# Kernel optimization log

Measured on AMD Instinct MI355X. Metric: run time of the kernel, lower is better.

The kernel has to match this reference:

```python
import jax, jax.numpy as jnp
import numpy as np

N = 50000       # nodes
E = 600000      # edges (avg degree 12)
F_IN = 64       # input_bands
F_HID = 128     # 2 * input_bands
F_OUT = 128     # output_bands
EPS = 1e-5      # BatchNorm eps


def setup_inputs() -> dict:
    key = jax.random.key(0)
    ks = jax.random.split(key, 12)
    x = jax.random.normal(ks[0], (N, F_IN), jnp.float32)
    edge_index = jax.random.randint(ks[1], (2, E), 0, N, dtype=jnp.int32)
    # GCNConv weight (glorot-ish) and bias
    W1 = jax.random.normal(ks[2], (F_IN, F_HID), jnp.float32) / np.sqrt(F_IN)
    b1 = jnp.zeros((F_HID,), jnp.float32)
    gamma1 = jnp.ones((F_HID,), jnp.float32)
    beta1 = jnp.zeros((F_HID,), jnp.float32)
    # SAGEConv: lin_l (aggregated neighbors, with bias), lin_r (root, no bias)
    Wl = jax.random.normal(ks[3], (F_HID, F_OUT), jnp.float32) / np.sqrt(F_HID)
    bl = jnp.zeros((F_OUT,), jnp.float32)
    Wr = jax.random.normal(ks[4], (F_HID, F_OUT), jnp.float32) / np.sqrt(F_HID)
    gamma2 = jnp.ones((F_OUT,), jnp.float32)
    beta2 = jnp.zeros((F_OUT,), jnp.float32)
    return {"x": x, "edge_index": edge_index, "W1": W1, "b1": b1,
            "gamma1": gamma1, "beta1": beta1, "Wl": Wl, "bl": bl,
            "Wr": Wr, "gamma2": gamma2, "beta2": beta2}


def _bn_train(h, gamma, beta):
    # BatchNorm1d in training mode: biased batch stats over the node axis
    mean = h.mean(axis=0)
    var = h.var(axis=0)
    return gamma * (h - mean) * jax.lax.rsqrt(var + EPS) + beta


def _gcn_conv(x, src, dst, W, b):
    # PyG GCNConv: x' = D^{-1/2}(A + I)D^{-1/2} X W + b
    h = x @ W                                   # [N, F_HID]
    loop = jnp.arange(N, dtype=src.dtype)
    src_sl = jnp.concatenate([src, loop])       # self-loops appended
    dst_sl = jnp.concatenate([dst, loop])
    deg = jax.ops.segment_sum(jnp.ones(E + N, h.dtype), dst_sl, num_segments=N)
    dis = jnp.where(deg > 0, jax.lax.rsqrt(deg), 0.0)  # deg^{-1/2}, inf -> 0
    norm = dis[src_sl] * dis[dst_sl]            # [E+N]
    msg = h[src_sl] * norm[:, None]             # gather + scale
    return jax.ops.segment_sum(msg, dst_sl, num_segments=N) + b


def _sage_conv(x, src, dst, Wl, bl, Wr):
    # PyG SAGEConv (mean aggr): x' = lin_l(mean_{j in N(i)} x_j) + lin_r(x_i)
    cnt = jax.ops.segment_sum(jnp.ones(E, x.dtype), dst, num_segments=N)
    neigh = jax.ops.segment_sum(x[src], dst, num_segments=N)
    neigh = neigh / jnp.maximum(cnt, 1.0)[:, None]
    return neigh @ Wl + bl + x @ Wr


def reference(x, edge_index, W1, b1, gamma1, beta1, Wl, bl, Wr, gamma2, beta2):
    src, dst = edge_index[0], edge_index[1]
    h = _gcn_conv(x, src, dst, W1, b1)
    h = jax.nn.relu(_bn_train(h, gamma1, beta1))  # dropout = identity (eval)
    h = _sage_conv(h, src, dst, Wl, bl, Wr)
    h = jax.nn.relu(_bn_train(h, gamma2, beta2))
    return h
```

## Files before the change

kernel.cpp:

```cpp
#include <hip/hip_runtime.h>

#define NN 50000
#define NE 600000
#define FIN 64
#define FHID 128
#define BN_EPS 1e-5f
#define CAP 64

typedef __attribute__((ext_vector_type(8))) short short8;
typedef __attribute__((ext_vector_type(4))) float f32x4;

__device__ __forceinline__ unsigned short f2bf(float f) {
  unsigned u = __float_as_uint(f);
  return (unsigned short)((u + 0x7FFFu + ((u >> 16) & 1u)) >> 16);
}
__device__ __forceinline__ float bfs(unsigned short u) {
  return __uint_as_float(((unsigned)u) << 16);
}
__device__ __forceinline__ float bflo(unsigned v) { return __uint_as_float(v << 16); }
__device__ __forceinline__ float bfhi(unsigned v) { return __uint_as_float(v & 0xFFFF0000u); }
__device__ __forceinline__ unsigned pk2(float lo, float hi) {
  return (unsigned)f2bf(lo) | ((unsigned)f2bf(hi) << 16);
}

__global__ __launch_bounds__(256) void bucket_fill(const int* __restrict__ src,
                                                   const int* __restrict__ dst,
                                                   int* __restrict__ cnt,
                                                   int* __restrict__ csr) {
  int e4 = blockIdx.x * 256 + threadIdx.x;
  if (e4 * 4 < NE) {
    int4 d4 = ((const int4*)dst)[e4];
    int4 s4 = ((const int4*)src)[e4];
    int p;
    p = atomicAdd(&cnt[d4.x], 1); if (p < CAP) csr[(size_t)d4.x * CAP + p] = s4.x;
    p = atomicAdd(&cnt[d4.y], 1); if (p < CAP) csr[(size_t)d4.y * CAP + p] = s4.y;
    p = atomicAdd(&cnt[d4.z], 1); if (p < CAP) csr[(size_t)d4.z * CAP + p] = s4.z;
    p = atomicAdd(&cnt[d4.w], 1); if (p < CAP) csr[(size_t)d4.w * CAP + p] = s4.w;
  }
}

__global__ __launch_bounds__(256) void scale_x(const float* __restrict__ x,
                                               const int* __restrict__ cnt,
                                               ushort4* __restrict__ xs,
                                               int* __restrict__ csr) {
  int i = blockIdx.x * 256 + threadIdx.x;
  float4 v = ((const float4*)x)[i];
  int node = i >> 4;
  float d = rsqrtf((float)(cnt[node] + 1));
  xs[i] = make_ushort4(f2bf(v.x * d), f2bf(v.y * d), f2bf(v.z * d), f2bf(v.w * d));
  if (i < NN) {
    int deg = min(cnt[i], CAP);
    int deg8 = (deg + 7) & ~7;
    int* cb = csr + (size_t)i * CAP;
    for (int p = deg; p < deg8; ++p) cb[p] = 0;
  }
}

__device__ __forceinline__ void gacc(float& a0, float& a1, float& a2, float& a3,
                                     ushort4 v) {
  a0 += bfs(v.x); a1 += bfs(v.y); a2 += bfs(v.z); a3 += bfs(v.w);
}

__global__ __launch_bounds__(256) void gcn_agg(const unsigned short* __restrict__ xs,
                                               const int* __restrict__ csr,
                                               const int* __restrict__ cnt,
                                               unsigned short* __restrict__ xa) {
  int tid = threadIdx.x;
  int node = blockIdx.x * 16 + (tid >> 4);
  int li = tid & 15;
  int degr = cnt[node];
  int deg = min(degr, CAP);
  int deg8 = (deg + 7) & ~7;
  float di = rsqrtf((float)(degr + 1));
  ushort4 sv = *(const ushort4*)(xs + (size_t)node * FIN + li * 4);
  float a0 = bfs(sv.x), a1 = bfs(sv.y), a2 = bfs(sv.z), a3 = bfs(sv.w);
  ushort4 zv = *(const ushort4*)(xs + li * 4);
  const int* cb = csr + (size_t)node * CAP;
  int4 sA = *(const int4*)(cb);
  int4 sB = *(const int4*)(cb + 4);
  for (int e = 0; e < deg8; e += 8) {
    int pn = min(e + 8, CAP - 8);
    int4 nA = *(const int4*)(cb + pn);
    int4 nB = *(const int4*)(cb + pn + 4);
    ushort4 v0 = *(const ushort4*)(xs + (size_t)sA.x * FIN + li * 4);
    ushort4 v1 = *(const ushort4*)(xs + (size_t)sA.y * FIN + li * 4);
    ushort4 v2 = *(const ushort4*)(xs + (size_t)sA.z * FIN + li * 4);
    ushort4 v3 = *(const ushort4*)(xs + (size_t)sA.w * FIN + li * 4);
    ushort4 v4 = *(const ushort4*)(xs + (size_t)sB.x * FIN + li * 4);
    ushort4 v5 = *(const ushort4*)(xs + (size_t)sB.y * FIN + li * 4);
    ushort4 v6 = *(const ushort4*)(xs + (size_t)sB.z * FIN + li * 4);
    ushort4 v7 = *(const ushort4*)(xs + (size_t)sB.w * FIN + li * 4);
    gacc(a0, a1, a2, a3, v0); gacc(a0, a1, a2, a3, v1);
    gacc(a0, a1, a2, a3, v2); gacc(a0, a1, a2, a3, v3);
    gacc(a0, a1, a2, a3, v4); gacc(a0, a1, a2, a3, v5);
    gacc(a0, a1, a2, a3, v6); gacc(a0, a1, a2, a3, v7);
    sA = nA; sB = nB;
  }
  float pc = (float)(deg8 - deg);
  a0 -= pc * bfs(zv.x); a1 -= pc * bfs(zv.y);
  a2 -= pc * bfs(zv.z); a3 -= pc * bfs(zv.w);
  ushort4 o = make_ushort4(f2bf(di * a0), f2bf(di * a1), f2bf(di * a2), f2bf(di * a3));
  *(ushort4*)(xa + (size_t)node * FIN + li * 4) = o;
}

__device__ __forceinline__ void sacc(float* a, uint4 v) {
  a[0] += bflo(v.x); a[1] += bfhi(v.x);
  a[2] += bflo(v.y); a[3] += bfhi(v.y);
  a[4] += bflo(v.z); a[5] += bfhi(v.z);
  a[6] += bflo(v.w); a[7] += bfhi(v.w);
}

__global__ __launch_bounds__(256) void sage_agg(const unsigned* __restrict__ hb,
                                                const int* __restrict__ csr,
                                                const int* __restrict__ cnt,
                                                unsigned* __restrict__ neighb) {
  int tid = threadIdx.x;
  int node = blockIdx.x * 16 + (tid >> 4);
  int li = tid & 15;
  int degr = cnt[node];
  int deg = min(degr, CAP);
  int deg8 = (deg + 7) & ~7;
  float a[8];
#pragma unroll
  for (int i = 0; i < 8; ++i) a[i] = 0.f;
  uint4 zv = *(const uint4*)(hb + li * 4);
  const int* cb = csr + (size_t)node * CAP;
  int4 sA = *(const int4*)(cb);
  int4 sB = *(const int4*)(cb + 4);
  for (int e = 0; e < deg8; e += 8) {
    int pn = min(e + 8, CAP - 8);
    int4 nA = *(const int4*)(cb + pn);
    int4 nB = *(const int4*)(cb + pn + 4);
    uint4 v0 = *(const uint4*)(hb + (size_t)sA.x * 64 + li * 4);
    uint4 v1 = *(const uint4*)(hb + (size_t)sA.y * 64 + li * 4);
    uint4 v2 = *(const uint4*)(hb + (size_t)sA.z * 64 + li * 4);
    uint4 v3 = *(const uint4*)(hb + (size_t)sA.w * 64 + li * 4);
    uint4 v4 = *(const uint4*)(hb + (size_t)sB.x * 64 + li * 4);
    uint4 v5 = *(const uint4*)(hb + (size_t)sB.y * 64 + li * 4);
    uint4 v6 = *(const uint4*)(hb + (size_t)sB.z * 64 + li * 4);
    uint4 v7 = *(const uint4*)(hb + (size_t)sB.w * 64 + li * 4);
    sacc(a, v0); sacc(a, v1); sacc(a, v2); sacc(a, v3);
    sacc(a, v4); sacc(a, v5); sacc(a, v6); sacc(a, v7);
    sA = nA; sB = nB;
  }
  float pc = (float)(deg8 - deg);
  a[0] -= pc * bflo(zv.x); a[1] -= pc * bfhi(zv.x);
  a[2] -= pc * bflo(zv.y); a[3] -= pc * bfhi(zv.y);
  a[4] -= pc * bflo(zv.z); a[5] -= pc * bfhi(zv.z);
  a[6] -= pc * bflo(zv.w); a[7] -= pc * bfhi(zv.w);
  float inv = 1.0f / fmaxf((float)degr, 1.0f);
  uint4 o;
  o.x = pk2(a[0] * inv, a[1] * inv);
  o.y = pk2(a[2] * inv, a[3] * inv);
  o.z = pk2(a[4] * inv, a[5] * inv);
  o.w = pk2(a[6] * inv, a[7] * inv);
  *(uint4*)(neighb + (size_t)node * 64 + li * 4) = o;
}

template <int K1, int K2, bool OUTBF>
__global__ __launch_bounds__(256) void gemm_mfma(const short* __restrict__ A1,
                                                 const short* __restrict__ A2,
                                                 const float* __restrict__ B1,
                                                 const float* __restrict__ B2,
                                                 const float* __restrict__ bias,
                                                 float* __restrict__ Cf,
                                                 unsigned short* __restrict__ Cb,
                                                 float* __restrict__ sums,
                                                 float* __restrict__ sumsq) {
  constexpr int KT = K1 + K2;
  constexpr int NK1 = K1 / 32;
  constexpr int NKS = KT / 32;
  __shared__ short Bp[8 * NKS * 64 * 8];
  __shared__ float lsum[128], lsq[128];
  int tid = threadIdx.x;
  if (tid < 128) { lsum[tid] = 0.f; lsq[tid] = 0.f; }
  for (int idx = tid; idx < KT * 32; idx += 256) {
    int k = idx >> 5, c4 = idx & 31;
    const float* Bsrc = (K2 == 0 || k < K1) ? (B1 + k * 128) : (B2 + (k - K1) * 128);
    float4 wv = *(const float4*)(Bsrc + c4 * 4);
    int ks = k >> 5, q = (k >> 3) & 3, kk = k & 7;
#pragma unroll
    for (int j = 0; j < 4; ++j) {
      int c = c4 * 4 + j;
      int nf = c >> 4, r = c & 15;
      float wj = j == 0 ? wv.x : (j == 1 ? wv.y : (j == 2 ? wv.z : wv.w));
      Bp[((nf * NKS + ks) * 64 + q * 16 + r) * 8 + kk] = (short)f2bf(wj);
    }
  }
  __syncthreads();

  int lane = tid & 63;
  int w = tid >> 6;
  int r = lane & 15;
  int q = lane >> 4;
  int row_base = blockIdx.x * 128 + w * 32;
  int row0 = row_base + r;
  int row1 = row_base + 16 + r;
  row0 = row0 < NN ? row0 : NN - 1;
  row1 = row1 < NN ? row1 : NN - 1;

  short8 af[2][NKS];
#pragma unroll
  for (int ks = 0; ks < NKS; ++ks) {
    const short* A = (K2 == 0 || ks < NK1) ? A1 : A2;
    const int Kw = (K2 == 0 || ks < NK1) ? K1 : K2;
    const int ko = ((K2 == 0 || ks < NK1) ? ks : ks - NK1) * 32;
    af[0][ks] = *(const short8*)(A + (size_t)row0 * Kw + ko + q * 8);
    af[1][ks] = *(const short8*)(A + (size_t)row1 * Kw + ko + q * 8);
  }

  f32x4 acc[2][8];
#pragma unroll
  for (int m = 0; m < 2; ++m)
#pragma unroll
    for (int n = 0; n < 8; ++n) acc[m][n] = (f32x4){0.f, 0.f, 0.f, 0.f};

#pragma unroll
  for (int ks = 0; ks < NKS; ++ks) {
#pragma unroll
    for (int n = 0; n < 8; ++n) {
      short8 bf = *(const short8*)(Bp + ((size_t)(n * NKS + ks) * 64 + lane) * 8);
      acc[0][n] = __builtin_amdgcn_mfma_f32_16x16x32_bf16(af[0][ks], bf, acc[0][n], 0, 0, 0);
      acc[1][n] = __builtin_amdgcn_mfma_f32_16x16x32_bf16(af[1][ks], bf, acc[1][n], 0, 0, 0);
    }
  }

  float bias_r[8];
#pragma unroll
  for (int n = 0; n < 8; ++n) bias_r[n] = bias[n * 16 + r];
  float cs[8], cq[8];
#pragma unroll
  for (int n = 0; n < 8; ++n) { cs[n] = 0.f; cq[n] = 0.f; }
#pragma unroll
  for (int m = 0; m < 2; ++m)
#pragma unroll
    for (int i = 0; i < 4; ++i) {
      int row = row_base + m * 16 + q * 4 + i;
      if (row < NN) {
#pragma unroll
        for (int n = 0; n < 8; ++n) {
          float v = acc[m][n][i] + bias_r[n];
          int col = n * 16 + r;
          if constexpr (OUTBF)
            Cb[(size_t)row * 128 + col] = f2bf(v);
          else
            Cf[(size_t)row * 128 + col] = v;
          cs[n] += v;
          cq[n] += v * v;
        }
      }
    }
#pragma unroll
  for (int n = 0; n < 8; ++n) {
    atomicAdd(&lsum[n * 16 + r], cs[n]);
    atomicAdd(&lsq[n * 16 + r], cq[n]);
  }
  __syncthreads();
  if (tid < 128) {
    atomicAdd(&sums[tid], lsum[tid]);
    atomicAdd(&sumsq[tid], lsq[tid]);
  }
}

__global__ __launch_bounds__(256) void bn_apply_bf(unsigned* __restrict__ hb,
                                                   const float* __restrict__ sums,
                                                   const float* __restrict__ sumsq,
                                                   const float* __restrict__ gamma,
                                                   const float* __restrict__ beta) {
  __shared__ float sc[128], sh[128];
  int t = threadIdx.x;
  if (t < 128) {
    float mean = sums[t] * (1.0f / NN);
    float var = fmaxf(sumsq[t] * (1.0f / NN) - mean * mean, 0.f);
    float inv = rsqrtf(var + BN_EPS);
    float s = gamma[t] * inv;
    sc[t] = s;
    sh[t] = beta[t] - mean * s;
  }
  __syncthreads();
  int i = blockIdx.x * 256 + t;
  uint2 v = ((uint2*)hb)[i];
  int c = (i & 31) * 4;
  float f0 = fmaxf(fmaf(bflo(v.x), sc[c + 0], sh[c + 0]), 0.f);
  float f1 = fmaxf(fmaf(bfhi(v.x), sc[c + 1], sh[c + 1]), 0.f);
  float f2 = fmaxf(fmaf(bflo(v.y), sc[c + 2], sh[c + 2]), 0.f);
  float f3 = fmaxf(fmaf(bfhi(v.y), sc[c + 3], sh[c + 3]), 0.f);
  v.x = (unsigned)f2bf(f0) | ((unsigned)f2bf(f1) << 16);
  v.y = (unsigned)f2bf(f2) | ((unsigned)f2bf(f3) << 16);
  ((uint2*)hb)[i] = v;
}

__global__ __launch_bounds__(256) void bn_apply_f32(float* __restrict__ out,
                                                    const float* __restrict__ sums,
                                                    const float* __restrict__ sumsq,
                                                    const float* __restrict__ gamma,
                                                    const float* __restrict__ beta) {
  __shared__ float sc[128], sh[128];
  int t = threadIdx.x;
  if (t < 128) {
    float mean = sums[t] * (1.0f / NN);
    float var = fmaxf(sumsq[t] * (1.0f / NN) - mean * mean, 0.f);
    float inv = rsqrtf(var + BN_EPS);
    float s = gamma[t] * inv;
    sc[t] = s;
    sh[t] = beta[t] - mean * s;
  }
  __syncthreads();
  int i4 = blockIdx.x * 256 + t;
  float4 v = ((const float4*)out)[i4];
  int f = (i4 & 31) * 4;
  v.x = fmaxf(fmaf(v.x, sc[f + 0], sh[f + 0]), 0.f);
  v.y = fmaxf(fmaf(v.y, sc[f + 1], sh[f + 1]), 0.f);
  v.z = fmaxf(fmaf(v.z, sc[f + 2], sh[f + 2]), 0.f);
  v.w = fmaxf(fmaf(v.w, sc[f + 3], sh[f + 3]), 0.f);
  ((float4*)out)[i4] = v;
}

extern "C" void kernel_launch(void* const* d_in, const int* in_sizes, int n_in,
                              void* d_out, int out_size, void* d_ws, size_t ws_size,
                              hipStream_t stream) {
  const float* x   = (const float*)d_in[0];
  const int*   ei  = (const int*)d_in[1];
  const float* W1  = (const float*)d_in[2];
  const float* b1  = (const float*)d_in[3];
  const float* g1  = (const float*)d_in[4];
  const float* be1 = (const float*)d_in[5];
  const float* Wl  = (const float*)d_in[6];
  const float* bl  = (const float*)d_in[7];
  const float* Wr  = (const float*)d_in[8];
  const float* g2  = (const float*)d_in[9];
  const float* be2 = (const float*)d_in[10];
  const int* srcp = ei;
  const int* dstp = ei + NE;

  char* w = (char*)d_ws;
  auto alloc = [&](size_t bytes) {
    char* p = w;
    w += (bytes + 255) & ~(size_t)255;
    return p;
  };
  int*   cnt     = (int*)alloc((size_t)NN * 4);
  int*   csr     = (int*)alloc((size_t)NN * CAP * 4);
  unsigned short* xs     = (unsigned short*)alloc((size_t)NN * FIN * 2);
  unsigned short* xa     = (unsigned short*)alloc((size_t)NN * FIN * 2);
  unsigned short* hb     = (unsigned short*)alloc((size_t)NN * FHID * 2);
  unsigned*       neighb = (unsigned*)alloc((size_t)NN * FHID * 2);
  float* stats   = (float*)alloc(8 * 128 * 4);
  float* sums1 = stats,       *sumsq1 = stats + 128;
  float* sums2 = stats + 512, *sumsq2 = stats + 640;

  hipMemsetAsync(cnt, 0, (size_t)NN * 4, stream);
  hipMemsetAsync(stats, 0, 8 * 128 * 4, stream);

  int nbE4 = (NE / 4 + 255) / 256;
  int nbA = NN / 16;
  int nbG = (NN + 127) / 128;

  bucket_fill<<<nbE4, 256, 0, stream>>>(srcp, dstp, cnt, csr);
  scale_x<<<NN * FIN / 4 / 256, 256, 0, stream>>>(x, cnt, (ushort4*)xs, csr);

  gcn_agg<<<nbA, 256, 0, stream>>>(xs, csr, cnt, xa);
  gemm_mfma<64, 0, true><<<nbG, 256, 0, stream>>>(
      (const short*)xa, nullptr, W1, nullptr, b1, nullptr, hb, sums1, sumsq1);
  bn_apply_bf<<<NN * FHID / 4 / 256, 256, 0, stream>>>((unsigned*)hb, sums1, sumsq1,
                                                       g1, be1);

  sage_agg<<<nbA, 256, 0, stream>>>((const unsigned*)hb, csr, cnt, neighb);
  gemm_mfma<128, 128, false><<<nbG, 256, 0, stream>>>(
      (const short*)neighb, (const short*)hb, Wl, Wr, bl, (float*)d_out, nullptr,
      sums2, sumsq2);
  bn_apply_f32<<<NN * FHID / 4 / 256, 256, 0, stream>>>((float*)d_out, sums2, sumsq2,
                                                        g2, be2);
}
```

Measured before the change: 234.6 us.

## Fuse preprocessing and BatchNorm apply into persistent kernels with grid barriers

Bucket fill, x scaling and GCN aggregation are merged into one persistent kernel of 768 blocks separated by software grid barriers. The BatchNorm apply step moves into the GEMM kernels, which keep accumulators in registers across a grid barrier and write normalized output once. The two memsets become one. This removes several launches and the extra read and write of hidden and output tensors, but relies on all blocks being co-resident (the GEMM grid of 391 blocks at two per CU), or it deadlocks.

```diff
diff --git a/kernel.cpp b/kernel.cpp
--- a/kernel.cpp
+++ b/kernel.cpp
@@ -23,12 +23,34 @@
   return (unsigned)f2bf(lo) | ((unsigned)f2bf(hi) << 16);
 }
 
-__global__ __launch_bounds__(256) void bucket_fill(const int* __restrict__ src,
-                                                   const int* __restrict__ dst,
-                                                   int* __restrict__ cnt,
-                                                   int* __restrict__ csr) {
-  int e4 = blockIdx.x * 256 + threadIdx.x;
-  if (e4 * 4 < NE) {
+__device__ __forceinline__ void gridbar(int* ctr, int target) {
+  __syncthreads();
+  if (threadIdx.x == 0) {
+    __threadfence();
+    __hip_atomic_fetch_add(ctr, 1, __ATOMIC_ACQ_REL, __HIP_MEMORY_SCOPE_AGENT);
+    while (__hip_atomic_load(ctr, __ATOMIC_ACQUIRE, __HIP_MEMORY_SCOPE_AGENT) <
+           target)
+      __builtin_amdgcn_s_sleep(4);
+    __threadfence();
+  }
+  __syncthreads();
+}
+
+__device__ __forceinline__ void gacc(float& a0, float& a1, float& a2, float& a3,
+                                     ushort4 v) {
+  a0 += bfs(v.x); a1 += bfs(v.y); a2 += bfs(v.z); a3 += bfs(v.w);
+}
+
+__global__ __launch_bounds__(256, 4) void fused_pre(
+    const int* __restrict__ src, const int* __restrict__ dst,
+    const float* __restrict__ x, int* __restrict__ cnt, int* __restrict__ csr,
+    ushort4* __restrict__ xs, unsigned short* __restrict__ xa,
+    int* __restrict__ bar) {
+  int tid = threadIdx.x;
+  int gtid = blockIdx.x * 256 + tid;
+  int gstride = gridDim.x * 256;
+
+  for (int e4 = gtid; e4 < NE / 4; e4 += gstride) {
     int4 d4 = ((const int4*)dst)[e4];
     int4 s4 = ((const int4*)src)[e4];
     int p;
@@ -37,70 +59,64 @@
     p = atomicAdd(&cnt[d4.z], 1); if (p < CAP) csr[(size_t)d4.z * CAP + p] = s4.z;
     p = atomicAdd(&cnt[d4.w], 1); if (p < CAP) csr[(size_t)d4.w * CAP + p] = s4.w;
   }
-}
-
-__global__ __launch_bounds__(256) void scale_x(const float* __restrict__ x,
-                                               const int* __restrict__ cnt,
-                                               ushort4* __restrict__ xs,
-                                               int* __restrict__ csr) {
-  int i = blockIdx.x * 256 + threadIdx.x;
-  float4 v = ((const float4*)x)[i];
-  int node = i >> 4;
-  float d = rsqrtf((float)(cnt[node] + 1));
-  xs[i] = make_ushort4(f2bf(v.x * d), f2bf(v.y * d), f2bf(v.z * d), f2bf(v.w * d));
-  if (i < NN) {
-    int deg = min(cnt[i], CAP);
-    int deg8 = (deg + 7) & ~7;
-    int* cb = csr + (size_t)i * CAP;
-    for (int p = deg; p < deg8; ++p) cb[p] = 0;
-  }
-}
-
-__device__ __forceinline__ void gacc(float& a0, float& a1, float& a2, float& a3,
-                                     ushort4 v) {
-  a0 += bfs(v.x); a1 += bfs(v.y); a2 += bfs(v.z); a3 += bfs(v.w);
-}
-
-__global__ __launch_bounds__(256) void gcn_agg(const unsigned short* __restrict__ xs,
-                                               const int* __restrict__ csr,
-                                               const int* __restrict__ cnt,
-                                               unsigned short* __restrict__ xa) {
-  int tid = threadIdx.x;
-  int node = blockIdx.x * 16 + (tid >> 4);
-  int li = tid & 15;
-  int degr = cnt[node];
-  int deg = min(degr, CAP);
-  int deg8 = (deg + 7) & ~7;
-  float di = rsqrtf((float)(degr + 1));
-  ushort4 sv = *(const ushort4*)(xs + (size_t)node * FIN + li * 4);
-  float a0 = bfs(sv.x), a1 = bfs(sv.y), a2 = bfs(sv.z), a3 = bfs(sv.w);
-  ushort4 zv = *(const ushort4*)(xs + li * 4);
-  const int* cb = csr + (size_t)node * CAP;
-  int4 sA = *(const int4*)(cb);
-  int4 sB = *(const int4*)(cb + 4);
-  for (int e = 0; e < deg8; e += 8) {
-    int pn = min(e + 8, CAP - 8);
-    int4 nA = *(const int4*)(cb + pn);
-    int4 nB = *(const int4*)(cb + pn + 4);
-    ushort4 v0 = *(const ushort4*)(xs + (size_t)sA.x * FIN + li * 4);
-    ushort4 v1 = *(const ushort4*)(xs + (size_t)sA.y * FIN + li * 4);
-    ushort4 v2 = *(const ushort4*)(xs + (size_t)sA.z * FIN + li * 4);
-    ushort4 v3 = *(const ushort4*)(xs + (size_t)sA.w * FIN + li * 4);
-    ushort4 v4 = *(const ushort4*)(xs + (size_t)sB.x * FIN + li * 4);
-    ushort4 v5 = *(const ushort4*)(xs + (size_t)sB.y * FIN + li * 4);
-    ushort4 v6 = *(const ushort4*)(xs + (size_t)sB.z * FIN + li * 4);
-    ushort4 v7 = *(const ushort4*)(xs + (size_t)sB.w * FIN + li * 4);
-    gacc(a0, a1, a2, a3, v0); gacc(a0, a1, a2, a3, v1);
-    gacc(a0, a1, a2, a3, v2); gacc(a0, a1, a2, a3, v3);
-    gacc(a0, a1, a2, a3, v4); gacc(a0, a1, a2, a3, v5);
-    gacc(a0, a1, a2, a3, v6); gacc(a0, a1, a2, a3, v7);
-    sA = nA; sB = nB;
-  }
-  float pc = (float)(deg8 - deg);
-  a0 -= pc * bfs(zv.x); a1 -= pc * bfs(zv.y);
-  a2 -= pc * bfs(zv.z); a3 -= pc * bfs(zv.w);
-  ushort4 o = make_ushort4(f2bf(di * a0), f2bf(di * a1), f2bf(di * a2), f2bf(di * a3));
-  *(ushort4*)(xa + (size_t)node * FIN + li * 4) = o;
+  gridbar(bar + 0, gridDim.x);
+
+  for (int i = gtid; i < NN * FIN / 4; i += gstride) {
+    float4 v = ((const float4*)x)[i];
+    int node = i >> 4;
+    float d = rsqrtf((float)(cnt[node] + 1));
+    xs[i] = make_ushort4(f2bf(v.x * d), f2bf(v.y * d), f2bf(v.z * d), f2bf(v.w * d));
+    if (i < NN) {
+      int deg = min(cnt[i], CAP);
+      int deg8 = (deg + 7) & ~7;
+      int* cb = csr + (size_t)i * CAP;
+      for (int p = deg; p < deg8; ++p) cb[p] = 0;
+    }
+  }
+  gridbar(bar + 1, gridDim.x);
+
+  {
+    const unsigned short* xsu = (const unsigned short*)xs;
+    int li = tid & 15;
+    int g0 = blockIdx.x * 16 + (tid >> 4);
+    int ngroups = gridDim.x * 16;
+    ushort4 zv = *(const ushort4*)(xsu + li * 4);
+    for (int node = g0; node < NN; node += ngroups) {
+      int degr = cnt[node];
+      int deg = min(degr, CAP);
+      int deg8 = (deg + 7) & ~7;
+      float di = rsqrtf((float)(degr + 1));
+      ushort4 sv = *(const ushort4*)(xsu + (size_t)node * FIN + li * 4);
+      float a0 = bfs(sv.x), a1 = bfs(sv.y), a2 = bfs(sv.z), a3 = bfs(sv.w);
+      const int* cb = csr + (size_t)node * CAP;
+      int4 sA = *(const int4*)(cb);
+      int4 sB = *(const int4*)(cb + 4);
+      for (int e = 0; e < deg8; e += 8) {
+        int pn = min(e + 8, CAP - 8);
+        int4 nA = *(const int4*)(cb + pn);
+        int4 nB = *(const int4*)(cb + pn + 4);
+        ushort4 v0 = *(const ushort4*)(xsu + (size_t)sA.x * FIN + li * 4);
+        ushort4 v1 = *(const ushort4*)(xsu + (size_t)sA.y * FIN + li * 4);
+        ushort4 v2 = *(const ushort4*)(xsu + (size_t)sA.z * FIN + li * 4);
+        ushort4 v3 = *(const ushort4*)(xsu + (size_t)sA.w * FIN + li * 4);
+        ushort4 v4 = *(const ushort4*)(xsu + (size_t)sB.x * FIN + li * 4);
+        ushort4 v5 = *(const ushort4*)(xsu + (size_t)sB.y * FIN + li * 4);
+        ushort4 v6 = *(const ushort4*)(xsu + (size_t)sB.z * FIN + li * 4);
+        ushort4 v7 = *(const ushort4*)(xsu + (size_t)sB.w * FIN + li * 4);
+        gacc(a0, a1, a2, a3, v0); gacc(a0, a1, a2, a3, v1);
+        gacc(a0, a1, a2, a3, v2); gacc(a0, a1, a2, a3, v3);
+        gacc(a0, a1, a2, a3, v4); gacc(a0, a1, a2, a3, v5);
+        gacc(a0, a1, a2, a3, v6); gacc(a0, a1, a2, a3, v7);
+        sA = nA; sB = nB;
+      }
+      float pc = (float)(deg8 - deg);
+      a0 -= pc * bfs(zv.x); a1 -= pc * bfs(zv.y);
+      a2 -= pc * bfs(zv.z); a3 -= pc * bfs(zv.w);
+      ushort4 o = make_ushort4(f2bf(di * a0), f2bf(di * a1), f2bf(di * a2),
+                               f2bf(di * a3));
+      *(ushort4*)(xa + (size_t)node * FIN + li * 4) = o;
+    }
+  }
 }
 
 __device__ __forceinline__ void sacc(float* a, uint4 v) {
@@ -158,15 +174,13 @@
 }
 
 template <int K1, int K2, bool OUTBF>
-__global__ __launch_bounds__(256) void gemm_mfma(const short* __restrict__ A1,
-                                                 const short* __restrict__ A2,
-                                                 const float* __restrict__ B1,
-                                                 const float* __restrict__ B2,
-                                                 const float* __restrict__ bias,
-                                                 float* __restrict__ Cf,
-                                                 unsigned short* __restrict__ Cb,
-                                                 float* __restrict__ sums,
-                                                 float* __restrict__ sumsq) {
+__global__ __launch_bounds__(256, 2) void gemm_bn(
+    const short* __restrict__ A1, const short* __restrict__ A2,
+    const float* __restrict__ B1, const float* __restrict__ B2,
+    const float* __restrict__ bias, float* __restrict__ Cf,
+    unsigned short* __restrict__ Cb, float* __restrict__ sums,
+    float* __restrict__ sumsq, const float* __restrict__ gamma,
+    const float* __restrict__ beta, int* __restrict__ bar, int nblk) {
   constexpr int KT = K1 + K2;
   constexpr int NK1 = K1 / 32;
   constexpr int NKS = KT / 32;
@@ -240,11 +254,7 @@
 #pragma unroll
         for (int n = 0; n < 8; ++n) {
           float v = acc[m][n][i] + bias_r[n];
-          int col = n * 16 + r;
-          if constexpr (OUTBF)
-            Cb[(size_t)row * 128 + col] = f2bf(v);
-          else
-            Cf[(size_t)row * 128 + col] = v;
+          acc[m][n][i] = v;
           cs[n] += v;
           cq[n] += v * v;
         }
@@ -260,60 +270,36 @@
     atomicAdd(&sums[tid], lsum[tid]);
     atomicAdd(&sumsq[tid], lsq[tid]);
   }
-}
-
-__global__ __launch_bounds__(256) void bn_apply_bf(unsigned* __restrict__ hb,
-                                                   const float* __restrict__ sums,
-                                                   const float* __restrict__ sumsq,
-                                                   const float* __restrict__ gamma,
-                                                   const float* __restrict__ beta) {
-  __shared__ float sc[128], sh[128];
-  int t = threadIdx.x;
-  if (t < 128) {
-    float mean = sums[t] * (1.0f / NN);
-    float var = fmaxf(sumsq[t] * (1.0f / NN) - mean * mean, 0.f);
+
+  gridbar(bar, nblk);
+
+  if (tid < 128) {
+    float mean = sums[tid] * (1.0f / NN);
+    float var = fmaxf(sumsq[tid] * (1.0f / NN) - mean * mean, 0.f);
     float inv = rsqrtf(var + BN_EPS);
-    float s = gamma[t] * inv;
-    sc[t] = s;
-    sh[t] = beta[t] - mean * s;
-  }
-  __syncthreads();
-  int i = blockIdx.x * 256 + t;
-  uint2 v = ((uint2*)hb)[i];
-  int c = (i & 31) * 4;
-  float f0 = fmaxf(fmaf(bflo(v.x), sc[c + 0], sh[c + 0]), 0.f);
-  float f1 = fmaxf(fmaf(bfhi(v.x), sc[c + 1], sh[c + 1]), 0.f);
-  float f2 = fmaxf(fmaf(bflo(v.y), sc[c + 2], sh[c + 2]), 0.f);
-  float f3 = fmaxf(fmaf(bfhi(v.y), sc[c + 3], sh[c + 3]), 0.f);
-  v.x = (unsigned)f2bf(f0) | ((unsigned)f2bf(f1) << 16);
-  v.y = (unsigned)f2bf(f2) | ((unsigned)f2bf(f3) << 16);
-  ((uint2*)hb)[i] = v;
-}
-
-__global__ __launch_bounds__(256) void bn_apply_f32(float* __restrict__ out,
-                                                    const float* __restrict__ sums,
-                                                    const float* __restrict__ sumsq,
-                                                    const float* __restrict__ gamma,
-                                                    const float* __restrict__ beta) {
-  __shared__ float sc[128], sh[128];
-  int t = threadIdx.x;
-  if (t < 128) {
-    float mean = sums[t] * (1.0f / NN);
-    float var = fmaxf(sumsq[t] * (1.0f / NN) - mean * mean, 0.f);
-    float inv = rsqrtf(var + BN_EPS);
-    float s = gamma[t] * inv;
-    sc[t] = s;
-    sh[t] = beta[t] - mean * s;
-  }
-  __syncthreads();
-  int i4 = blockIdx.x * 256 + t;
-  float4 v = ((const float4*)out)[i4];
-  int f = (i4 & 31) * 4;
-  v.x = fmaxf(fmaf(v.x, sc[f + 0], sh[f + 0]), 0.f);
-  v.y = fmaxf(fmaf(v.y, sc[f + 1], sh[f + 1]), 0.f);
-  v.z = fmaxf(fmaf(v.z, sc[f + 2], sh[f + 2]), 0.f);
-  v.w = fmaxf(fmaf(v.w, sc[f + 3], sh[f + 3]), 0.f);
-  ((float4*)out)[i4] = v;
+    float s = gamma[tid] * inv;
+    lsum[tid] = s;
+    lsq[tid] = beta[tid] - mean * s;
+  }
+  __syncthreads();
+
+#pragma unroll
+  for (int m = 0; m < 2; ++m)
+#pragma unroll
+    for (int i = 0; i < 4; ++i) {
+      int row = row_base + m * 16 + q * 4 + i;
+      if (row < NN) {
+#pragma unroll
+        for (int n = 0; n < 8; ++n) {
+          int col = n * 16 + r;
+          float o = fmaxf(fmaf(acc[m][n][i], lsum[col], lsq[col]), 0.f);
+          if constexpr (OUTBF)
+            Cb[(size_t)row * 128 + col] = f2bf(o);
+          else
+            Cf[(size_t)row * 128 + col] = o;
+        }
+      }
+    }
 }
 
 extern "C" void kernel_launch(void* const* d_in, const int* in_sizes, int n_in,
@@ -339,36 +325,34 @@
     w += (bytes + 255) & ~(size_t)255;
     return p;
   };
-  int*   cnt     = (int*)alloc((size_t)NN * 4);
+  size_t zbytes = (8 + NN + 1024) * 4;
+  char* zz = (char*)alloc(zbytes);
+  int*   bar   = (int*)zz;
+  int*   cnt   = bar + 8;
+  float* stats = (float*)(cnt + NN);
+  float* sums1 = stats,       *sumsq1 = stats + 128;
+  float* sums2 = stats + 512, *sumsq2 = stats + 640;
+
   int*   csr     = (int*)alloc((size_t)NN * CAP * 4);
   unsigned short* xs     = (unsigned short*)alloc((size_t)NN * FIN * 2);
   unsigned short* xa     = (unsigned short*)alloc((size_t)NN * FIN * 2);
   unsigned short* hb     = (unsigned short*)alloc((size_t)NN * FHID * 2);
   unsigned*       neighb = (unsigned*)alloc((size_t)NN * FHID * 2);
-  float* stats   = (float*)alloc(8 * 128 * 4);
-  float* sums1 = stats,       *sumsq1 = stats + 128;
-  float* sums2 = stats + 512, *sumsq2 = stats + 640;
-
-  hipMemsetAsync(cnt, 0, (size_t)NN * 4, stream);
-  hipMemsetAsync(stats, 0, 8 * 128 * 4, stream);
-
-  int nbE4 = (NE / 4 + 255) / 256;
+
+  hipMemsetAsync(zz, 0, zbytes, stream);
+
   int nbA = NN / 16;
   int nbG = (NN + 127) / 128;
 
-  bucket_fill<<<nbE4, 256, 0, stream>>>(srcp, dstp, cnt, csr);
-  scale_x<<<NN * FIN / 4 / 256, 256, 0, stream>>>(x, cnt, (ushort4*)xs, csr);
-
-  gcn_agg<<<nbA, 256, 0, stream>>>(xs, csr, cnt, xa);
-  gemm_mfma<64, 0, true><<<nbG, 256, 0, stream>>>(
-      (const short*)xa, nullptr, W1, nullptr, b1, nullptr, hb, sums1, sumsq1);
-  bn_apply_bf<<<NN * FHID / 4 / 256, 256, 0, stream>>>((unsigned*)hb, sums1, sumsq1,
-                                                       g1, be1);
+  fused_pre<<<768, 256, 0, stream>>>(srcp, dstp, x, cnt, csr, (ushort4*)xs, xa, bar);
+
+  gemm_bn<64, 0, true><<<nbG, 256, 0, stream>>>(
+      (const short*)xa, nullptr, W1, nullptr, b1, nullptr, hb, sums1, sumsq1,
+      g1, be1, bar + 2, nbG);
 
   sage_agg<<<nbA, 256, 0, stream>>>((const unsigned*)hb, csr, cnt, neighb);
-  gemm_mfma<128, 128, false><<<nbG, 256, 0, stream>>>(
+
+  gemm_bn<128, 128, false><<<nbG, 256, 0, stream>>>(
       (const short*)neighb, (const short*)hb, Wl, Wr, bl, (float*)d_out, nullptr,
-      sums2, sumsq2);
-  bn_apply_f32<<<NN * FHID / 4 / 256, 256, 0, stream>>>((float*)d_out, sums2, sumsq2,
-                                                        g2, be2);
-}
+      sums2, sumsq2, g2, be2, bar + 3, nbG);
+}
```

Measured after the change: 542.7 us. 131% more time.
